# Performance work log

Hardware: AMD Instinct MI355X
Metric: run time of the kernel (lower is better)

## Reference

```python
import jax, jax.numpy as jnp
import numpy as np

EMBED_DIM = 384
N_DOCS = 262144
BATCH = 64
TOP_K = 8
EPS = 1e-8


def setup_inputs() -> dict:
    key = jax.random.key(0)
    kq, kd = jax.random.split(key)
    query = jax.random.normal(kq, (BATCH, EMBED_DIM), dtype=jnp.float32)
    doc_embeddings = jax.random.normal(kd, (N_DOCS, EMBED_DIM), dtype=jnp.float32)
    return {"query": query, "doc_embeddings": doc_embeddings, "top_k": TOP_K}


def reference(query, doc_embeddings, top_k):
    # Cosine similarity: L2-normalize both sides.
    qn = query / (jnp.linalg.norm(query, axis=-1, keepdims=True) + EPS)          # [B, d]
    dn = doc_embeddings / (jnp.linalg.norm(doc_embeddings, axis=-1, keepdims=True) + EPS)  # [N, d]
    # Similarity scores between every query and every document.
    scores = jnp.einsum('bd,nd->bn', qn, dn)                                      # [B, N]
    # Top-k retrieval.
    topk_scores, topk_idx = jax.lax.top_k(scores, top_k)                          # [B, k]
    # Gather retrieved document embeddings.
    retrieved = dn[topk_idx]                                                      # [B, k, d]
    # Context fusion: softmax-weighted sum of retrieved docs.
    weights = jax.nn.softmax(topk_scores, axis=-1)                                # [B, k]
    fused = jnp.einsum('bk,bkd->bd', weights, retrieved)                          # [B, d]
    return fused, topk_scores, topk_idx
```

## Files before the change

kernel.cpp:

```cpp
#include <hip/hip_runtime.h>
#include <math.h>


#define EMBED 384
#define NDOCS 262144
#define BATCH 64
#define TOPK 8
#define DBLK 128
#define NBLK (NDOCS / DBLK)
#define EPSN 1e-8f
#define SC_STRIDE 132

typedef __attribute__((ext_vector_type(8))) short bf16x8;
typedef __attribute__((ext_vector_type(4))) float f32x4;

#define INS8(s_, i_) do {                                                     \
    if ((s_) > ts[7] || ((s_) == ts[7] && (i_) < ti[7])) {                    \
        ts[7] = (s_); ti[7] = (i_);                                           \
        _Pragma("unroll")                                                     \
        for (int r_ = 7; r_ > 0; --r_) {                                      \
            bool sw_ = (ts[r_] > ts[r_-1]) ||                                 \
                       (ts[r_] == ts[r_-1] && ti[r_] < ti[r_-1]);             \
            float a_ = ts[r_-1]; int b_ = ti[r_-1];                           \
            ts[r_-1] = sw_ ? ts[r_] : a_;  ti[r_-1] = sw_ ? ti[r_] : b_;      \
            ts[r_]   = sw_ ? a_ : ts[r_];  ti[r_]   = sw_ ? b_ : ti[r_];      \
        }                                                                     \
    }                                                                         \
} while (0)

__device__ __forceinline__ void split8(float4 f0, float4 f1, bf16x8& bh, bf16x8& bl) {
    float f[8] = {f0.x, f0.y, f0.z, f0.w, f1.x, f1.y, f1.z, f1.w};
#pragma unroll
    for (int i = 0; i < 8; ++i) {
        unsigned u = __float_as_uint(f[i]);
        unsigned h = (u + 0x7fffu + ((u >> 16) & 1u)) >> 16;
        float fh = __uint_as_float(h << 16);
        float r = f[i] - fh;
        unsigned v = __float_as_uint(r);
        unsigned lo = (v + 0x7fffu + ((v >> 16) & 1u)) >> 16;
        bh[i] = (short)h;
        bl[i] = (short)lo;
    }
}

__device__ __forceinline__ float dot8(float4 f0, float4 f1, float s) {
    s = fmaf(f0.x, f0.x, s); s = fmaf(f0.y, f0.y, s);
    s = fmaf(f0.z, f0.z, s); s = fmaf(f0.w, f0.w, s);
    s = fmaf(f1.x, f1.x, s); s = fmaf(f1.y, f1.y, s);
    s = fmaf(f1.z, f1.z, s); s = fmaf(f1.w, f1.w, s);
    return s;
}

__global__ void qprep_kernel(const float* __restrict__ q,
                             unsigned short* __restrict__ qh,
                             unsigned short* __restrict__ ql) {
    const int row = blockIdx.x;
    const int lane = threadIdx.x;
    float v[6];
    float s = 0.f;
#pragma unroll
    for (int i = 0; i < 6; ++i) {
        v[i] = q[row * EMBED + lane + 64 * i];
        s = fmaf(v[i], v[i], s);
    }
#pragma unroll
    for (int off = 32; off > 0; off >>= 1) s += __shfl_xor(s, off);
    float rinv = 1.0f / (sqrtf(s) + EPSN);
#pragma unroll
    for (int i = 0; i < 6; ++i) {
        float f = v[i] * rinv;
        unsigned u = __float_as_uint(f);
        unsigned h = (u + 0x7fffu + ((u >> 16) & 1u)) >> 16;
        float fh = __uint_as_float(h << 16);
        float r = f - fh;
        unsigned vv = __float_as_uint(r);
        unsigned lo = (vv + 0x7fffu + ((vv >> 16) & 1u)) >> 16;
        qh[row * EMBED + lane + 64 * i] = (unsigned short)h;
        ql[row * EMBED + lane + 64 * i] = (unsigned short)lo;
    }
}

__global__ __launch_bounds__(256, 4) void score_topk_kernel(
        const float* __restrict__ docs,
        const unsigned short* __restrict__ qh,
        const unsigned short* __restrict__ ql,
        float* __restrict__ pscore, int* __restrict__ pidx) {
    __shared__ float S[BATCH * SC_STRIDE];

    const int tid = threadIdx.x;
    const int l = tid & 63;
    const int w = tid >> 6;
    const int rowl = l & 15;
    const int koff = (l >> 4) * 8;
    const int d0 = blockIdx.x * DBLK;

    f32x4 acc[2][4];
#pragma unroll
    for (int s = 0; s < 2; ++s)
#pragma unroll
        for (int m = 0; m < 4; ++m) acc[s][m] = (f32x4){0.f, 0.f, 0.f, 0.f};
    float sq0 = 0.f, sq1 = 0.f;

    const float* dp0 = docs + (size_t)(d0 + w * 32 + rowl) * EMBED + koff;
    const float* dp1 = dp0 + 16 * EMBED;
    const unsigned short* qhb = qh + rowl * EMBED + koff;
    const unsigned short* qlb = ql + rowl * EMBED + koff;

    float4 c00 = *(const float4*)dp0, c01 = *(const float4*)(dp0 + 4);
    float4 c10 = *(const float4*)dp1, c11 = *(const float4*)(dp1 + 4);

#define KBODY(kk, PREFETCH)                                                   \
    do {                                                                      \
        bf16x8 ah[4], al[4];                                                  \
        _Pragma("unroll")                                                     \
        for (int m = 0; m < 4; ++m) {                                         \
            ah[m] = *(const bf16x8*)(qhb + m * (16 * EMBED) + (kk));          \
            al[m] = *(const bf16x8*)(qlb + m * (16 * EMBED) + (kk));          \
        }                                                                     \
        float4 n00, n01, n10, n11;                                            \
        if (PREFETCH) {                                                       \
            n00 = *(const float4*)(dp0 + (kk) + 32);                          \
            n01 = *(const float4*)(dp0 + (kk) + 36);                          \
            n10 = *(const float4*)(dp1 + (kk) + 32);                          \
            n11 = *(const float4*)(dp1 + (kk) + 36);                          \
        }                                                                     \
        sq0 = dot8(c00, c01, sq0);                                            \
        sq1 = dot8(c10, c11, sq1);                                            \
        bf16x8 bh0, bl0, bh1, bl1;                                            \
        split8(c00, c01, bh0, bl0);                                           \
        split8(c10, c11, bh1, bl1);                                           \
        _Pragma("unroll")                                                     \
        for (int m = 0; m < 4; ++m)                                           \
            acc[0][m] = __builtin_amdgcn_mfma_f32_16x16x32_bf16(ah[m], bh0, acc[0][m], 0, 0, 0); \
        _Pragma("unroll")                                                     \
        for (int m = 0; m < 4; ++m)                                           \
            acc[1][m] = __builtin_amdgcn_mfma_f32_16x16x32_bf16(ah[m], bh1, acc[1][m], 0, 0, 0); \
        _Pragma("unroll")                                                     \
        for (int m = 0; m < 4; ++m)                                           \
            acc[0][m] = __builtin_amdgcn_mfma_f32_16x16x32_bf16(al[m], bh0, acc[0][m], 0, 0, 0); \
        _Pragma("unroll")                                                     \
        for (int m = 0; m < 4; ++m)                                           \
            acc[1][m] = __builtin_amdgcn_mfma_f32_16x16x32_bf16(al[m], bh1, acc[1][m], 0, 0, 0); \
        _Pragma("unroll")                                                     \
        for (int m = 0; m < 4; ++m)                                           \
            acc[0][m] = __builtin_amdgcn_mfma_f32_16x16x32_bf16(ah[m], bl0, acc[0][m], 0, 0, 0); \
        _Pragma("unroll")                                                     \
        for (int m = 0; m < 4; ++m)                                           \
            acc[1][m] = __builtin_amdgcn_mfma_f32_16x16x32_bf16(ah[m], bl1, acc[1][m], 0, 0, 0); \
        if (PREFETCH) { c00 = n00; c01 = n01; c10 = n10; c11 = n11; }         \
    } while (0)

#pragma unroll 1
    for (int kb = 0; kb < 11; ++kb) {
        KBODY(kb * 32, 1);
    }
    KBODY(352, 0);
#undef KBODY

    {
        float t0 = sq0;
        t0 += __shfl_xor(t0, 16);
        t0 += __shfl_xor(t0, 32);
        float rn0 = 1.0f / (sqrtf(t0) + EPSN);
        float t1 = sq1;
        t1 += __shfl_xor(t1, 16);
        t1 += __shfl_xor(t1, 32);
        float rn1 = 1.0f / (sqrtf(t1) + EPSN);
        const int q0 = (l >> 4) * 4;
#pragma unroll
        for (int m = 0; m < 4; ++m) {
            f32x4 a = acc[0][m];
            const int col0 = w * 32 + rowl;
            S[(m * 16 + q0 + 0) * SC_STRIDE + col0] = a[0] * rn0;
            S[(m * 16 + q0 + 1) * SC_STRIDE + col0] = a[1] * rn0;
            S[(m * 16 + q0 + 2) * SC_STRIDE + col0] = a[2] * rn0;
            S[(m * 16 + q0 + 3) * SC_STRIDE + col0] = a[3] * rn0;
            f32x4 b = acc[1][m];
            const int col1 = w * 32 + 16 + rowl;
            S[(m * 16 + q0 + 0) * SC_STRIDE + col1] = b[0] * rn1;
            S[(m * 16 + q0 + 1) * SC_STRIDE + col1] = b[1] * rn1;
            S[(m * 16 + q0 + 2) * SC_STRIDE + col1] = b[2] * rn1;
            S[(m * 16 + q0 + 3) * SC_STRIDE + col1] = b[3] * rn1;
        }
    }
    __syncthreads();

    float ts[8]; int ti[8];
#pragma unroll
    for (int r = 0; r < 8; ++r) { ts[r] = -3.402823466e38f; ti[r] = 0x7fffffff; }
    const int sq_ = tid & 63, half = tid >> 6;
    if (tid < 128) {
        for (int ii = 0; ii < 64; ++ii) {
            int d = half * 64 + ((ii + sq_) & 63);
            float sc = S[sq_ * SC_STRIDE + d];
            INS8(sc, d0 + d);
        }
    }
    __syncthreads();
    if (half == 1 && tid < 128) {
#pragma unroll
        for (int r = 0; r < 8; ++r) {
            S[sq_ * 8 + r] = ts[r];
            S[512 + sq_ * 8 + r] = __int_as_float(ti[r]);
        }
    }
    __syncthreads();
    if (tid < 64) {
#pragma unroll
        for (int r = 0; r < 8; ++r) {
            float s2 = S[sq_ * 8 + r];
            int i2 = __float_as_int(S[512 + sq_ * 8 + r]);
            INS8(s2, i2);
        }
        size_t o = ((size_t)sq_ * NBLK + blockIdx.x) * TOPK;
        *(float4*)&pscore[o]     = make_float4(ts[0], ts[1], ts[2], ts[3]);
        *(float4*)&pscore[o + 4] = make_float4(ts[4], ts[5], ts[6], ts[7]);
        *(int4*)&pidx[o]     = make_int4(ti[0], ti[1], ti[2], ti[3]);
        *(int4*)&pidx[o + 4] = make_int4(ti[4], ti[5], ti[6], ti[7]);
    }
}

__global__ __launch_bounds__(256) void merge_fuse_kernel(
        const float* __restrict__ docs, const float* __restrict__ pscore,
        const int* __restrict__ pidx, float* __restrict__ out) {
    const int q = blockIdx.x;
    const int tid = threadIdx.x;
    __shared__ float ls[2048];
    __shared__ int   li[2048];
    __shared__ float ls2[512];
    __shared__ int   li2[512];
    __shared__ float ls3[64];
    __shared__ int   li3[64];
    __shared__ int   fi[TOPK];
    __shared__ float wr[TOPK];

    const float* sp = pscore + (size_t)q * (NBLK * TOPK);
    const int*   ip = pidx   + (size_t)q * (NBLK * TOPK);

    float ts[8]; int ti[8];
#pragma unroll
    for (int r = 0; r < 8; ++r) { ts[r] = -3.402823466e38f; ti[r] = 0x7fffffff; }

    for (int i = 0; i < 16; ++i) {
        int c4 = tid + (i << 8);
        float4 s = ((const float4*)sp)[c4];
        if (s.x >= ts[7] || s.y >= ts[7] || s.z >= ts[7] || s.w >= ts[7]) {
            int4 iv = ((const int4*)ip)[c4];
            INS8(s.x, iv.x); INS8(s.y, iv.y); INS8(s.z, iv.z); INS8(s.w, iv.w);
        }
    }
#pragma unroll
    for (int r = 0; r < 8; ++r) { ls[tid * 8 + r] = ts[r]; li[tid * 8 + r] = ti[r]; }
    __syncthreads();

    if (tid < 64) {
#pragma unroll
        for (int r = 0; r < 8; ++r) { ts[r] = -3.402823466e38f; ti[r] = 0x7fffffff; }
        for (int c = 0; c < 32; ++c) {
            int e = tid + c * 64;
            float s = ls[e]; int gi = li[e];
            INS8(s, gi);
        }
#pragma unroll
        for (int r = 0; r < 8; ++r) { ls2[tid * 8 + r] = ts[r]; li2[tid * 8 + r] = ti[r]; }
    }
    __syncthreads();

    if (tid < 8) {
#pragma unroll
        for (int r = 0; r < 8; ++r) { ts[r] = -3.402823466e38f; ti[r] = 0x7fffffff; }
        for (int c = 0; c < 64; ++c) {
            int e = tid + c * 8;
            float s = ls2[e]; int gi = li2[e];
            INS8(s, gi);
        }
#pragma unroll
        for (int r = 0; r < 8; ++r) { ls3[tid * 8 + r] = ts[r]; li3[tid * 8 + r] = ti[r]; }
    }
    __syncthreads();

    if (tid == 0) {
#pragma unroll
        for (int r = 0; r < 8; ++r) { ts[r] = -3.402823466e38f; ti[r] = 0x7fffffff; }
        for (int e = 0; e < 64; ++e) {
            float s = ls3[e]; int gi = li3[e];
            INS8(s, gi);
        }
        float m = ts[0];
        float w[8]; float sum = 0.f;
#pragma unroll
        for (int r = 0; r < 8; ++r) { w[r] = expf(ts[r] - m); sum += w[r]; }
        float rs = 1.0f / sum;
#pragma unroll
        for (int r = 0; r < 8; ++r) {
            fi[r] = ti[r];
            wr[r] = w[r] * rs;
            out[BATCH * EMBED + q * TOPK + r] = ts[r];
            out[BATCH * EMBED + BATCH * TOPK + q * TOPK + r] = (float)ti[r];
        }
    }
    __syncthreads();

    int lane = tid & 63, wave = tid >> 6;
    for (int r = wave; r < TOPK; r += 4) {
        const float* dp = docs + (size_t)fi[r] * EMBED;
        float s = 0.f;
#pragma unroll
        for (int i = 0; i < 6; ++i) { float v = dp[lane + 64 * i]; s = fmaf(v, v, s); }
#pragma unroll
        for (int off = 32; off > 0; off >>= 1) s += __shfl_xor(s, off);
        if (lane == 0) wr[r] = wr[r] / (sqrtf(s) + EPSN);
    }
    __syncthreads();

    for (int dim = tid; dim < EMBED; dim += 256) {
        float a = 0.f;
#pragma unroll
        for (int r = 0; r < 8; ++r)
            a += wr[r] * docs[(size_t)fi[r] * EMBED + dim];
        out[q * EMBED + dim] = a;
    }
}

extern "C" void kernel_launch(void* const* d_in, const int* in_sizes, int n_in,
                              void* d_out, int out_size, void* d_ws, size_t ws_size,
                              hipStream_t stream) {
    const float* query = (const float*)d_in[0];
    const float* docs  = (const float*)d_in[1];
    float* out = (float*)d_out;

    char* ws = (char*)d_ws;
    unsigned short* qh = (unsigned short*)ws;
    unsigned short* ql = (unsigned short*)(ws + 49152);
    float* pscore = (float*)(ws + 98304);
    int*   pidx   = (int*)(ws + 98304 + (size_t)NBLK * BATCH * TOPK * 4);

    qprep_kernel<<<64, 64, 0, stream>>>(query, qh, ql);
    score_topk_kernel<<<NBLK, 256, 0, stream>>>(docs, qh, ql, pscore, pidx);
    merge_fuse_kernel<<<BATCH, 256, 0, stream>>>(docs, pscore, pidx, out);
}
```

Before: 288.1 us.

## Stage doc tiles via async global-to-LDS loads and split top-k merge

The score kernel now streams document tiles into a double-buffered, XOR-swizzled LDS region with global_load_lds. Explicit vmcnt waits let the next k-slice load overlap the split and MFMA work on the current one, and query fragments are fetched with inline-asm global loads. The merge is split into two kernels: 512 blocks each reduce a chunk of partial top-k lists, then a small kernel does the final merge and the weighted fusion. This adds parallelism to the merge stage but costs an extra launch. The hand-tuned waitcnt values and the larger LDS footprint may limit occupancy or correctness if the counts are wrong.

New measurement: 277.7 us. 3.6% less time.

```diff
diff --git a/kernel.cpp b/kernel.cpp
--- a/kernel.cpp
+++ b/kernel.cpp
@@ -28,8 +28,8 @@
     }                                                                         \
 } while (0)
 
-__device__ __forceinline__ void split8(float4 f0, float4 f1, bf16x8& bh, bf16x8& bl) {
-    float f[8] = {f0.x, f0.y, f0.z, f0.w, f1.x, f1.y, f1.z, f1.w};
+__device__ __forceinline__ void split8v(f32x4 f0, f32x4 f1, bf16x8& bh, bf16x8& bl) {
+    float f[8] = {f0[0], f0[1], f0[2], f0[3], f1[0], f1[1], f1[2], f1[3]};
 #pragma unroll
     for (int i = 0; i < 8; ++i) {
         unsigned u = __float_as_uint(f[i]);
@@ -43,12 +43,24 @@
     }
 }
 
-__device__ __forceinline__ float dot8(float4 f0, float4 f1, float s) {
-    s = fmaf(f0.x, f0.x, s); s = fmaf(f0.y, f0.y, s);
-    s = fmaf(f0.z, f0.z, s); s = fmaf(f0.w, f0.w, s);
-    s = fmaf(f1.x, f1.x, s); s = fmaf(f1.y, f1.y, s);
-    s = fmaf(f1.z, f1.z, s); s = fmaf(f1.w, f1.w, s);
+__device__ __forceinline__ float dot8v(f32x4 f0, f32x4 f1, float s) {
+#pragma unroll
+    for (int i = 0; i < 4; ++i) s = fmaf(f0[i], f0[i], s);
+#pragma unroll
+    for (int i = 0; i < 4; ++i) s = fmaf(f1[i], f1[i], s);
     return s;
+}
+
+__device__ __forceinline__ int4 gload16(const void* p) {
+    int4 r;
+    asm volatile("global_load_dwordx4 %0, %1, off" : "=v"(r) : "v"(p) : "memory");
+    return r;
+}
+
+__device__ __forceinline__ f32x4 dsread16(unsigned a) {
+    f32x4 r;
+    asm volatile("ds_read_b128 %0, %1" : "=v"(r) : "v"(a) : "memory");
+    return r;
 }
 
 __global__ void qprep_kernel(const float* __restrict__ q,
@@ -85,13 +97,13 @@
         const unsigned short* __restrict__ qh,
         const unsigned short* __restrict__ ql,
         float* __restrict__ pscore, int* __restrict__ pidx) {
-    __shared__ float S[BATCH * SC_STRIDE];
+    __shared__ __align__(16) char smem[34816];
 
     const int tid = threadIdx.x;
     const int l = tid & 63;
-    const int w = tid >> 6;
+    const int wv = tid >> 6;
     const int rowl = l & 15;
-    const int koff = (l >> 4) * 8;
+    const int ksub = l >> 4;
     const int d0 = blockIdx.x * DBLK;
 
     f32x4 acc[2][4];
@@ -101,62 +113,75 @@
         for (int m = 0; m < 4; ++m) acc[s][m] = (f32x4){0.f, 0.f, 0.f, 0.f};
     float sq0 = 0.f, sq1 = 0.f;
 
-    const float* dp0 = docs + (size_t)(d0 + w * 32 + rowl) * EMBED + koff;
-    const float* dp1 = dp0 + 16 * EMBED;
-    const unsigned short* qhb = qh + rowl * EMBED + koff;
-    const unsigned short* qlb = ql + rowl * EMBED + koff;
-
-    float4 c00 = *(const float4*)dp0, c01 = *(const float4*)(dp0 + 4);
-    float4 c10 = *(const float4*)dp1, c11 = *(const float4*)(dp1 + 4);
-
-#define KBODY(kk, PREFETCH)                                                   \
-    do {                                                                      \
-        bf16x8 ah[4], al[4];                                                  \
-        _Pragma("unroll")                                                     \
-        for (int m = 0; m < 4; ++m) {                                         \
-            ah[m] = *(const bf16x8*)(qhb + m * (16 * EMBED) + (kk));          \
-            al[m] = *(const bf16x8*)(qlb + m * (16 * EMBED) + (kk));          \
-        }                                                                     \
-        float4 n00, n01, n10, n11;                                            \
-        if (PREFETCH) {                                                       \
-            n00 = *(const float4*)(dp0 + (kk) + 32);                          \
-            n01 = *(const float4*)(dp0 + (kk) + 36);                          \
-            n10 = *(const float4*)(dp1 + (kk) + 32);                          \
-            n11 = *(const float4*)(dp1 + (kk) + 36);                          \
-        }                                                                     \
-        sq0 = dot8(c00, c01, sq0);                                            \
-        sq1 = dot8(c10, c11, sq1);                                            \
-        bf16x8 bh0, bl0, bh1, bl1;                                            \
-        split8(c00, c01, bh0, bl0);                                           \
-        split8(c10, c11, bh1, bl1);                                           \
-        _Pragma("unroll")                                                     \
-        for (int m = 0; m < 4; ++m)                                           \
-            acc[0][m] = __builtin_amdgcn_mfma_f32_16x16x32_bf16(ah[m], bh0, acc[0][m], 0, 0, 0); \
-        _Pragma("unroll")                                                     \
-        for (int m = 0; m < 4; ++m)                                           \
-            acc[1][m] = __builtin_amdgcn_mfma_f32_16x16x32_bf16(ah[m], bh1, acc[1][m], 0, 0, 0); \
-        _Pragma("unroll")                                                     \
-        for (int m = 0; m < 4; ++m)                                           \
-            acc[0][m] = __builtin_amdgcn_mfma_f32_16x16x32_bf16(al[m], bh0, acc[0][m], 0, 0, 0); \
-        _Pragma("unroll")                                                     \
-        for (int m = 0; m < 4; ++m)                                           \
-            acc[1][m] = __builtin_amdgcn_mfma_f32_16x16x32_bf16(al[m], bh1, acc[1][m], 0, 0, 0); \
-        _Pragma("unroll")                                                     \
-        for (int m = 0; m < 4; ++m)                                           \
-            acc[0][m] = __builtin_amdgcn_mfma_f32_16x16x32_bf16(ah[m], bl0, acc[0][m], 0, 0, 0); \
-        _Pragma("unroll")                                                     \
-        for (int m = 0; m < 4; ++m)                                           \
-            acc[1][m] = __builtin_amdgcn_mfma_f32_16x16x32_bf16(ah[m], bl1, acc[1][m], 0, 0, 0); \
-        if (PREFETCH) { c00 = n00; c01 = n01; c10 = n10; c11 = n11; }         \
-    } while (0)
+    const float* sgsrc = docs + (size_t)(d0 + wv * 32 + (l >> 3)) * EMBED
+                              + (((l & 7) ^ (l >> 3)) << 2);
+    const unsigned short* qhb = qh + rowl * EMBED + ksub * 8;
+    const unsigned short* qlb = ql + rowl * EMBED + ksub * 8;
+
+    const unsigned bufb = (unsigned)(uintptr_t)smem;
+    const unsigned off00 = wv * 4096 + rowl * 128 + ((ksub * 32 +  0) ^ ((rowl & 7) << 4));
+    const unsigned off01 = wv * 4096 + rowl * 128 + ((ksub * 32 + 16) ^ ((rowl & 7) << 4));
+    const unsigned off10 = off00 + 2048;
+    const unsigned off11 = off01 + 2048;
+
+    {
+        float* db = (float*)smem + wv * 1024;
+#pragma unroll
+        for (int j = 0; j < 4; ++j)
+            __builtin_amdgcn_global_load_lds(sgsrc + j * 3072, db + j * 256, 16, 0, 0);
+    }
+
+#define SCORE_ITER(KB, DO_STAGE, VM1, VM2)                                     \
+    {                                                                          \
+        int4 qr[8];                                                            \
+        _Pragma("unroll")                                                      \
+        for (int m = 0; m < 4; ++m) {                                          \
+            qr[m]     = gload16(qhb + m * (16 * EMBED) + (KB) * 32);           \
+            qr[4 + m] = gload16(qlb + m * (16 * EMBED) + (KB) * 32);           \
+        }                                                                      \
+        if (DO_STAGE) {                                                        \
+            float* db = (float*)(smem + (((KB) + 1) & 1) * 16384) + wv * 1024; \
+            _Pragma("unroll")                                                  \
+            for (int j = 0; j < 4; ++j)                                        \
+                __builtin_amdgcn_global_load_lds(                              \
+                    sgsrc + j * 3072 + ((KB) + 1) * 32, db + j * 256, 16, 0, 0);\
+        }                                                                      \
+        asm volatile("s_waitcnt " VM1 ::: "memory");                           \
+        unsigned pb = bufb + ((KB) & 1) * 16384;                               \
+        f32x4 d00 = dsread16(pb + off00);                                      \
+        f32x4 d01 = dsread16(pb + off01);                                      \
+        f32x4 d10 = dsread16(pb + off10);                                      \
+        f32x4 d11 = dsread16(pb + off11);                                      \
+        asm volatile("s_waitcnt " VM2 " lgkmcnt(0)" ::: "memory");             \
+        __builtin_amdgcn_sched_barrier(0);                                     \
+        sq0 = dot8v(d00, d01, sq0);                                            \
+        sq1 = dot8v(d10, d11, sq1);                                            \
+        bf16x8 bh0, bl0, bh1, bl1;                                             \
+        split8v(d00, d01, bh0, bl0);                                           \
+        split8v(d10, d11, bh1, bl1);                                           \
+        _Pragma("unroll")                                                      \
+        for (int m = 0; m < 4; ++m) {                                          \
+            bf16x8 ah = *(bf16x8*)&qr[m];                                      \
+            bf16x8 al = *(bf16x8*)&qr[4 + m];                                  \
+            acc[0][m] = __builtin_amdgcn_mfma_f32_16x16x32_bf16(ah, bh0, acc[0][m], 0, 0, 0); \
+            acc[1][m] = __builtin_amdgcn_mfma_f32_16x16x32_bf16(ah, bh1, acc[1][m], 0, 0, 0); \
+            acc[0][m] = __builtin_amdgcn_mfma_f32_16x16x32_bf16(al, bh0, acc[0][m], 0, 0, 0); \
+            acc[1][m] = __builtin_amdgcn_mfma_f32_16x16x32_bf16(al, bh1, acc[1][m], 0, 0, 0); \
+            acc[0][m] = __builtin_amdgcn_mfma_f32_16x16x32_bf16(ah, bl0, acc[0][m], 0, 0, 0); \
+            acc[1][m] = __builtin_amdgcn_mfma_f32_16x16x32_bf16(ah, bl1, acc[1][m], 0, 0, 0); \
+        }                                                                      \
+    }
 
 #pragma unroll 1
     for (int kb = 0; kb < 11; ++kb) {
-        KBODY(kb * 32, 1);
-    }
-    KBODY(352, 0);
-#undef KBODY
-
+        SCORE_ITER(kb, 1, "vmcnt(12)", "vmcnt(4)")
+    }
+    SCORE_ITER(11, 0, "vmcnt(8)", "vmcnt(0)")
+#undef SCORE_ITER
+
+    __syncthreads();
+
+    float* S = (float*)smem;
     {
         float t0 = sq0;
         t0 += __shfl_xor(t0, 16);
@@ -166,17 +191,17 @@
         t1 += __shfl_xor(t1, 16);
         t1 += __shfl_xor(t1, 32);
         float rn1 = 1.0f / (sqrtf(t1) + EPSN);
-        const int q0 = (l >> 4) * 4;
+        const int q0 = ksub * 4;
+        const int col0 = wv * 32 + rowl;
+        const int col1 = col0 + 16;
 #pragma unroll
         for (int m = 0; m < 4; ++m) {
             f32x4 a = acc[0][m];
-            const int col0 = w * 32 + rowl;
             S[(m * 16 + q0 + 0) * SC_STRIDE + col0] = a[0] * rn0;
             S[(m * 16 + q0 + 1) * SC_STRIDE + col0] = a[1] * rn0;
             S[(m * 16 + q0 + 2) * SC_STRIDE + col0] = a[2] * rn0;
             S[(m * 16 + q0 + 3) * SC_STRIDE + col0] = a[3] * rn0;
             f32x4 b = acc[1][m];
-            const int col1 = w * 32 + 16 + rowl;
             S[(m * 16 + q0 + 0) * SC_STRIDE + col1] = b[0] * rn1;
             S[(m * 16 + q0 + 1) * SC_STRIDE + col1] = b[1] * rn1;
             S[(m * 16 + q0 + 2) * SC_STRIDE + col1] = b[2] * rn1;
@@ -220,10 +245,11 @@
     }
 }
 
-__global__ __launch_bounds__(256) void merge_fuse_kernel(
-        const float* __restrict__ docs, const float* __restrict__ pscore,
-        const int* __restrict__ pidx, float* __restrict__ out) {
-    const int q = blockIdx.x;
+__global__ __launch_bounds__(256) void merge_a_kernel(
+        const float* __restrict__ pscore, const int* __restrict__ pidx,
+        float* __restrict__ cs, int* __restrict__ ci) {
+    const int q = blockIdx.x >> 3;
+    const int c = blockIdx.x & 7;
     const int tid = threadIdx.x;
     __shared__ float ls[2048];
     __shared__ int   li[2048];
@@ -231,59 +257,76 @@
     __shared__ int   li2[512];
     __shared__ float ls3[64];
     __shared__ int   li3[64];
-    __shared__ int   fi[TOPK];
-    __shared__ float wr[TOPK];
-
-    const float* sp = pscore + (size_t)q * (NBLK * TOPK);
-    const int*   ip = pidx   + (size_t)q * (NBLK * TOPK);
+
+    {
+        size_t o = ((size_t)q * NBLK + c * 256 + tid) * TOPK;
+        float4 s0 = *(const float4*)&pscore[o];
+        float4 s1 = *(const float4*)&pscore[o + 4];
+        int4 i0 = *(const int4*)&pidx[o];
+        int4 i1 = *(const int4*)&pidx[o + 4];
+        ls[tid * 8 + 0] = s0.x; ls[tid * 8 + 1] = s0.y;
+        ls[tid * 8 + 2] = s0.z; ls[tid * 8 + 3] = s0.w;
+        ls[tid * 8 + 4] = s1.x; ls[tid * 8 + 5] = s1.y;
+        ls[tid * 8 + 6] = s1.z; ls[tid * 8 + 7] = s1.w;
+        li[tid * 8 + 0] = i0.x; li[tid * 8 + 1] = i0.y;
+        li[tid * 8 + 2] = i0.z; li[tid * 8 + 3] = i0.w;
+        li[tid * 8 + 4] = i1.x; li[tid * 8 + 5] = i1.y;
+        li[tid * 8 + 6] = i1.z; li[tid * 8 + 7] = i1.w;
+    }
+    __syncthreads();
 
     float ts[8]; int ti[8];
-#pragma unroll
-    for (int r = 0; r < 8; ++r) { ts[r] = -3.402823466e38f; ti[r] = 0x7fffffff; }
-
-    for (int i = 0; i < 16; ++i) {
-        int c4 = tid + (i << 8);
-        float4 s = ((const float4*)sp)[c4];
-        if (s.x >= ts[7] || s.y >= ts[7] || s.z >= ts[7] || s.w >= ts[7]) {
-            int4 iv = ((const int4*)ip)[c4];
-            INS8(s.x, iv.x); INS8(s.y, iv.y); INS8(s.z, iv.z); INS8(s.w, iv.w);
-        }
-    }
-#pragma unroll
-    for (int r = 0; r < 8; ++r) { ls[tid * 8 + r] = ts[r]; li[tid * 8 + r] = ti[r]; }
-    __syncthreads();
-
     if (tid < 64) {
 #pragma unroll
         for (int r = 0; r < 8; ++r) { ts[r] = -3.402823466e38f; ti[r] = 0x7fffffff; }
-        for (int c = 0; c < 32; ++c) {
-            int e = tid + c * 64;
-            float s = ls[e]; int gi = li[e];
+        for (int e = 0; e < 32; ++e) {
+            int k = tid + e * 64;
+            float s = ls[k]; int gi = li[k];
             INS8(s, gi);
         }
 #pragma unroll
         for (int r = 0; r < 8; ++r) { ls2[tid * 8 + r] = ts[r]; li2[tid * 8 + r] = ti[r]; }
     }
     __syncthreads();
-
     if (tid < 8) {
 #pragma unroll
         for (int r = 0; r < 8; ++r) { ts[r] = -3.402823466e38f; ti[r] = 0x7fffffff; }
-        for (int c = 0; c < 64; ++c) {
-            int e = tid + c * 8;
-            float s = ls2[e]; int gi = li2[e];
+        for (int e = 0; e < 64; ++e) {
+            int k = tid + e * 8;
+            float s = ls2[k]; int gi = li2[k];
             INS8(s, gi);
         }
 #pragma unroll
         for (int r = 0; r < 8; ++r) { ls3[tid * 8 + r] = ts[r]; li3[tid * 8 + r] = ti[r]; }
     }
     __syncthreads();
-
     if (tid == 0) {
 #pragma unroll
         for (int r = 0; r < 8; ++r) { ts[r] = -3.402823466e38f; ti[r] = 0x7fffffff; }
         for (int e = 0; e < 64; ++e) {
             float s = ls3[e]; int gi = li3[e];
+            INS8(s, gi);
+        }
+        size_t o = (size_t)(q * 8 + c) * TOPK;
+#pragma unroll
+        for (int r = 0; r < 8; ++r) { cs[o + r] = ts[r]; ci[o + r] = ti[r]; }
+    }
+}
+
+__global__ __launch_bounds__(256) void merge_b_kernel(
+        const float* __restrict__ docs, const float* __restrict__ cs,
+        const int* __restrict__ ci, float* __restrict__ out) {
+    const int q = blockIdx.x;
+    const int tid = threadIdx.x;
+    __shared__ int   fi[TOPK];
+    __shared__ float wr[TOPK];
+
+    if (tid == 0) {
+        float ts[8]; int ti[8];
+#pragma unroll
+        for (int r = 0; r < 8; ++r) { ts[r] = -3.402823466e38f; ti[r] = 0x7fffffff; }
+        for (int e = 0; e < 64; ++e) {
+            float s = cs[q * 64 + e]; int gi = ci[q * 64 + e];
             INS8(s, gi);
         }
         float m = ts[0];
@@ -334,8 +377,12 @@
     unsigned short* ql = (unsigned short*)(ws + 49152);
     float* pscore = (float*)(ws + 98304);
     int*   pidx   = (int*)(ws + 98304 + (size_t)NBLK * BATCH * TOPK * 4);
+    char*  ws3    = ws + 98304 + 2 * (size_t)NBLK * BATCH * TOPK * 4;
+    float* cs     = (float*)ws3;
+    int*   ci     = (int*)(ws3 + BATCH * 8 * TOPK * 4);
 
     qprep_kernel<<<64, 64, 0, stream>>>(query, qh, ql);
     score_topk_kernel<<<NBLK, 256, 0, stream>>>(docs, qh, ql, pscore, pidx);
-    merge_fuse_kernel<<<BATCH, 256, 0, stream>>>(docs, pscore, pidx, out);
-}
+    merge_a_kernel<<<BATCH * 8, 256, 0, stream>>>(pscore, pidx, cs, ci);
+    merge_b_kernel<<<BATCH, 256, 0, stream>>>(docs, cs, ci, out);
+}
```

## Score in single bf16 from pre-swizzled doc copy, rescore top candidates in fp32

Applied to the files above, without the earlier changes.

Replaces the three-term split-bf16 MFMA scoring with a single bf16×bf16 pass. A new conversion kernel first writes docs as a bf16 copy in an MFMA-friendly tiled layout, and the score kernel reads that copy. The merge kernel now keeps 256 candidates per query (top 16 from each of 16 chunks), recomputes their exact fp32 cosine scores from the original docs, and selects the final top-8 from those. This cuts MFMA and conversion work in the hot scoring loop, but adds a full read of the fp32 docs plus a write of a 200MB bf16 copy on every call. It also risks missing true top-k documents if bf16 error pushes them out of the 16-per-block candidate set.

Result: slower. 425.8 us (+47.8%).

```diff
diff --git a/kernel.cpp b/kernel.cpp
--- a/kernel.cpp
+++ b/kernel.cpp
@@ -6,10 +6,9 @@
 #define NDOCS 262144
 #define BATCH 64
 #define TOPK 8
-#define DBLK 128
-#define NBLK (NDOCS / DBLK)
+#define NBLK 2048
 #define EPSN 1e-8f
-#define SC_STRIDE 132
+#define SCW 132
 
 typedef __attribute__((ext_vector_type(8))) short bf16x8;
 typedef __attribute__((ext_vector_type(4))) float f32x4;
@@ -28,32 +27,28 @@
     }                                                                         \
 } while (0)
 
-__device__ __forceinline__ void split8(float4 f0, float4 f1, bf16x8& bh, bf16x8& bl) {
-    float f[8] = {f0.x, f0.y, f0.z, f0.w, f1.x, f1.y, f1.z, f1.w};
-#pragma unroll
-    for (int i = 0; i < 8; ++i) {
-        unsigned u = __float_as_uint(f[i]);
-        unsigned h = (u + 0x7fffu + ((u >> 16) & 1u)) >> 16;
-        float fh = __uint_as_float(h << 16);
-        float r = f[i] - fh;
-        unsigned v = __float_as_uint(r);
-        unsigned lo = (v + 0x7fffu + ((v >> 16) & 1u)) >> 16;
-        bh[i] = (short)h;
-        bl[i] = (short)lo;
-    }
-}
-
-__device__ __forceinline__ float dot8(float4 f0, float4 f1, float s) {
-    s = fmaf(f0.x, f0.x, s); s = fmaf(f0.y, f0.y, s);
-    s = fmaf(f0.z, f0.z, s); s = fmaf(f0.w, f0.w, s);
-    s = fmaf(f1.x, f1.x, s); s = fmaf(f1.y, f1.y, s);
-    s = fmaf(f1.z, f1.z, s); s = fmaf(f1.w, f1.w, s);
-    return s;
+#define INS16(s_, i_) do {                                                    \
+    if ((s_) > ts[15] || ((s_) == ts[15] && (i_) < ti[15])) {                 \
+        ts[15] = (s_); ti[15] = (i_);                                         \
+        _Pragma("unroll")                                                     \
+        for (int r_ = 15; r_ > 0; --r_) {                                     \
+            bool sw_ = (ts[r_] > ts[r_-1]) ||                                 \
+                       (ts[r_] == ts[r_-1] && ti[r_] < ti[r_-1]);             \
+            float a_ = ts[r_-1]; int b_ = ti[r_-1];                           \
+            ts[r_-1] = sw_ ? ts[r_] : a_;  ti[r_-1] = sw_ ? ti[r_] : b_;      \
+            ts[r_]   = sw_ ? a_ : ts[r_];  ti[r_]   = sw_ ? b_ : ti[r_];      \
+        }                                                                     \
+    }                                                                         \
+} while (0)
+
+__device__ __forceinline__ unsigned rne1(float f) {
+    unsigned u = __float_as_uint(f);
+    return (u + 0x7fffu + ((u >> 16) & 1u)) >> 16;
 }
 
 __global__ void qprep_kernel(const float* __restrict__ q,
-                             unsigned short* __restrict__ qh,
-                             unsigned short* __restrict__ ql) {
+                             float* __restrict__ qn,
+                             unsigned short* __restrict__ qhf) {
     const int row = blockIdx.x;
     const int lane = threadIdx.x;
     float v[6];
@@ -68,94 +63,85 @@
     float rinv = 1.0f / (sqrtf(s) + EPSN);
 #pragma unroll
     for (int i = 0; i < 6; ++i) {
+        int k = lane + 64 * i;
         float f = v[i] * rinv;
-        unsigned u = __float_as_uint(f);
-        unsigned h = (u + 0x7fffu + ((u >> 16) & 1u)) >> 16;
-        float fh = __uint_as_float(h << 16);
-        float r = f - fh;
-        unsigned vv = __float_as_uint(r);
-        unsigned lo = (vv + 0x7fffu + ((vv >> 16) & 1u)) >> 16;
-        qh[row * EMBED + lane + 64 * i] = (unsigned short)h;
-        ql[row * EMBED + lane + 64 * i] = (unsigned short)lo;
+        qn[row * EMBED + k] = f;
+        qhf[(row >> 4) * 6144 + (k >> 5) * 512 + ((k >> 3) & 3) * 128
+            + (row & 15) * 8 + (k & 7)] = (unsigned short)rne1(f);
+    }
+}
+
+__global__ __launch_bounds__(256) void conv_kernel(
+        const float* __restrict__ docs, unsigned short* __restrict__ T) {
+    __shared__ __align__(16) uint4 L4[1536];
+    uint2* L2p = (uint2*)L4;
+    const int tid = threadIdx.x;
+
+    for (int p4 = 0; p4 < 4; ++p4) {
+        const int panel = blockIdx.x * 4 + p4;
+        const float4* src = (const float4*)docs + (size_t)panel * 3072;
+        if (p4) __syncthreads();
+#pragma unroll
+        for (int i = 0; i < 12; ++i) {
+            int F = i * 256 + tid;
+            float4 v = src[F];
+            int dd = (F * 10923) >> 20;
+            int r4 = F - dd * 96;
+            uint2 hv;
+            hv.x = rne1(v.x) | (rne1(v.y) << 16);
+            hv.y = rne1(v.z) | (rne1(v.w) << 16);
+            unsigned byte_off = (unsigned)((r4 >> 3) * 2048 + (dd >> 4) * 1024
+                              + ((r4 >> 1) & 3) * 256 + (dd & 15) * 16
+                              + (r4 & 1) * 8);
+            L2p[byte_off >> 3] = hv;
+        }
+        __syncthreads();
+        uint4* dst = (uint4*)((char*)T + (size_t)panel * 24576);
+#pragma unroll
+        for (int j = 0; j < 6; ++j)
+            dst[j * 256 + tid] = L4[j * 256 + tid];
     }
 }
 
 __global__ __launch_bounds__(256, 4) void score_topk_kernel(
-        const float* __restrict__ docs,
-        const unsigned short* __restrict__ qh,
-        const unsigned short* __restrict__ ql,
+        const unsigned short* __restrict__ T,
+        const unsigned short* __restrict__ qhf,
         float* __restrict__ pscore, int* __restrict__ pidx) {
-    __shared__ float S[BATCH * SC_STRIDE];
+    __shared__ float S[BATCH * SCW];
 
     const int tid = threadIdx.x;
     const int l = tid & 63;
     const int w = tid >> 6;
-    const int rowl = l & 15;
-    const int koff = (l >> 4) * 8;
-    const int d0 = blockIdx.x * DBLK;
+    const int d0 = blockIdx.x * 128;
+
+    const char* Tb = (const char*)T + (size_t)(blockIdx.x * 4 + w) * 24576 + l * 16;
+    const char* Qb = (const char*)qhf + l * 16;
 
     f32x4 acc[2][4];
 #pragma unroll
-    for (int s = 0; s < 2; ++s)
-#pragma unroll
-        for (int m = 0; m < 4; ++m) acc[s][m] = (f32x4){0.f, 0.f, 0.f, 0.f};
+    for (int dt = 0; dt < 2; ++dt)
+#pragma unroll
+        for (int qt = 0; qt < 4; ++qt) acc[dt][qt] = (f32x4){0.f, 0.f, 0.f, 0.f};
     float sq0 = 0.f, sq1 = 0.f;
 
-    const float* dp0 = docs + (size_t)(d0 + w * 32 + rowl) * EMBED + koff;
-    const float* dp1 = dp0 + 16 * EMBED;
-    const unsigned short* qhb = qh + rowl * EMBED + koff;
-    const unsigned short* qlb = ql + rowl * EMBED + koff;
-
-    float4 c00 = *(const float4*)dp0, c01 = *(const float4*)(dp0 + 4);
-    float4 c10 = *(const float4*)dp1, c11 = *(const float4*)(dp1 + 4);
-
-#define KBODY(kk, PREFETCH)                                                   \
-    do {                                                                      \
-        bf16x8 ah[4], al[4];                                                  \
-        _Pragma("unroll")                                                     \
-        for (int m = 0; m < 4; ++m) {                                         \
-            ah[m] = *(const bf16x8*)(qhb + m * (16 * EMBED) + (kk));          \
-            al[m] = *(const bf16x8*)(qlb + m * (16 * EMBED) + (kk));          \
-        }                                                                     \
-        float4 n00, n01, n10, n11;                                            \
-        if (PREFETCH) {                                                       \
-            n00 = *(const float4*)(dp0 + (kk) + 32);                          \
-            n01 = *(const float4*)(dp0 + (kk) + 36);                          \
-            n10 = *(const float4*)(dp1 + (kk) + 32);                          \
-            n11 = *(const float4*)(dp1 + (kk) + 36);                          \
-        }                                                                     \
-        sq0 = dot8(c00, c01, sq0);                                            \
-        sq1 = dot8(c10, c11, sq1);                                            \
-        bf16x8 bh0, bl0, bh1, bl1;                                            \
-        split8(c00, c01, bh0, bl0);                                           \
-        split8(c10, c11, bh1, bl1);                                           \
-        _Pragma("unroll")                                                     \
-        for (int m = 0; m < 4; ++m)                                           \
-            acc[0][m] = __builtin_amdgcn_mfma_f32_16x16x32_bf16(ah[m], bh0, acc[0][m], 0, 0, 0); \
-        _Pragma("unroll")                                                     \
-        for (int m = 0; m < 4; ++m)                                           \
-            acc[1][m] = __builtin_amdgcn_mfma_f32_16x16x32_bf16(ah[m], bh1, acc[1][m], 0, 0, 0); \
-        _Pragma("unroll")                                                     \
-        for (int m = 0; m < 4; ++m)                                           \
-            acc[0][m] = __builtin_amdgcn_mfma_f32_16x16x32_bf16(al[m], bh0, acc[0][m], 0, 0, 0); \
-        _Pragma("unroll")                                                     \
-        for (int m = 0; m < 4; ++m)                                           \
-            acc[1][m] = __builtin_amdgcn_mfma_f32_16x16x32_bf16(al[m], bh1, acc[1][m], 0, 0, 0); \
-        _Pragma("unroll")                                                     \
-        for (int m = 0; m < 4; ++m)                                           \
-            acc[0][m] = __builtin_amdgcn_mfma_f32_16x16x32_bf16(ah[m], bl0, acc[0][m], 0, 0, 0); \
-        _Pragma("unroll")                                                     \
-        for (int m = 0; m < 4; ++m)                                           \
-            acc[1][m] = __builtin_amdgcn_mfma_f32_16x16x32_bf16(ah[m], bl1, acc[1][m], 0, 0, 0); \
-        if (PREFETCH) { c00 = n00; c01 = n01; c10 = n10; c11 = n11; }         \
-    } while (0)
-
-#pragma unroll 1
-    for (int kb = 0; kb < 11; ++kb) {
-        KBODY(kb * 32, 1);
-    }
-    KBODY(352, 0);
-#undef KBODY
+#pragma unroll
+    for (int kb = 0; kb < 12; ++kb) {
+        bf16x8 b0 = *(const bf16x8*)(Tb + kb * 2048);
+        bf16x8 b1 = *(const bf16x8*)(Tb + kb * 2048 + 1024);
+#pragma unroll
+        for (int e = 0; e < 8; ++e) {
+            float f0 = __uint_as_float(((unsigned)(unsigned short)b0[e]) << 16);
+            float f1 = __uint_as_float(((unsigned)(unsigned short)b1[e]) << 16);
+            sq0 = fmaf(f0, f0, sq0);
+            sq1 = fmaf(f1, f1, sq1);
+        }
+#pragma unroll
+        for (int qt = 0; qt < 4; ++qt) {
+            bf16x8 a = *(const bf16x8*)(Qb + qt * 12288 + kb * 1024);
+            acc[0][qt] = __builtin_amdgcn_mfma_f32_16x16x32_bf16(a, b0, acc[0][qt], 0, 0, 0);
+            acc[1][qt] = __builtin_amdgcn_mfma_f32_16x16x32_bf16(a, b1, acc[1][qt], 0, 0, 0);
+        }
+    }
 
     {
         float t0 = sq0;
@@ -167,20 +153,20 @@
         t1 += __shfl_xor(t1, 32);
         float rn1 = 1.0f / (sqrtf(t1) + EPSN);
         const int q0 = (l >> 4) * 4;
-#pragma unroll
-        for (int m = 0; m < 4; ++m) {
-            f32x4 a = acc[0][m];
-            const int col0 = w * 32 + rowl;
-            S[(m * 16 + q0 + 0) * SC_STRIDE + col0] = a[0] * rn0;
-            S[(m * 16 + q0 + 1) * SC_STRIDE + col0] = a[1] * rn0;
-            S[(m * 16 + q0 + 2) * SC_STRIDE + col0] = a[2] * rn0;
-            S[(m * 16 + q0 + 3) * SC_STRIDE + col0] = a[3] * rn0;
-            f32x4 b = acc[1][m];
-            const int col1 = w * 32 + 16 + rowl;
-            S[(m * 16 + q0 + 0) * SC_STRIDE + col1] = b[0] * rn1;
-            S[(m * 16 + q0 + 1) * SC_STRIDE + col1] = b[1] * rn1;
-            S[(m * 16 + q0 + 2) * SC_STRIDE + col1] = b[2] * rn1;
-            S[(m * 16 + q0 + 3) * SC_STRIDE + col1] = b[3] * rn1;
+        const int col0 = w * 32 + (l & 15);
+        const int col1 = col0 + 16;
+#pragma unroll
+        for (int qt = 0; qt < 4; ++qt) {
+            f32x4 a = acc[0][qt];
+            S[(qt * 16 + q0 + 0) * SCW + col0] = a[0] * rn0;
+            S[(qt * 16 + q0 + 1) * SCW + col0] = a[1] * rn0;
+            S[(qt * 16 + q0 + 2) * SCW + col0] = a[2] * rn0;
+            S[(qt * 16 + q0 + 3) * SCW + col0] = a[3] * rn0;
+            f32x4 b = acc[1][qt];
+            S[(qt * 16 + q0 + 0) * SCW + col1] = b[0] * rn1;
+            S[(qt * 16 + q0 + 1) * SCW + col1] = b[1] * rn1;
+            S[(qt * 16 + q0 + 2) * SCW + col1] = b[2] * rn1;
+            S[(qt * 16 + q0 + 3) * SCW + col1] = b[3] * rn1;
         }
     }
     __syncthreads();
@@ -192,7 +178,7 @@
     if (tid < 128) {
         for (int ii = 0; ii < 64; ++ii) {
             int d = half * 64 + ((ii + sq_) & 63);
-            float sc = S[sq_ * SC_STRIDE + d];
+            float sc = S[sq_ * SCW + d];
             INS8(sc, d0 + d);
         }
     }
@@ -220,96 +206,115 @@
     }
 }
 
-__global__ __launch_bounds__(256) void merge_fuse_kernel(
-        const float* __restrict__ docs, const float* __restrict__ pscore,
-        const int* __restrict__ pidx, float* __restrict__ out) {
+__global__ __launch_bounds__(256) void rescore_kernel(
+        const float* __restrict__ docs, const float* __restrict__ qn,
+        const float* __restrict__ pscore, const int* __restrict__ pidx,
+        float* __restrict__ out) {
     const int q = blockIdx.x;
     const int tid = threadIdx.x;
-    __shared__ float ls[2048];
-    __shared__ int   li[2048];
-    __shared__ float ls2[512];
-    __shared__ int   li2[512];
-    __shared__ float ls3[64];
-    __shared__ int   li3[64];
+    __shared__ float s1[4096];
+    __shared__ int   i1[4096];
+    __shared__ int   cand[256];
+    __shared__ float cs2[256];
+    __shared__ float cn2[256];
     __shared__ int   fi[TOPK];
     __shared__ float wr[TOPK];
 
-    const float* sp = pscore + (size_t)q * (NBLK * TOPK);
-    const int*   ip = pidx   + (size_t)q * (NBLK * TOPK);
-
-    float ts[8]; int ti[8];
-#pragma unroll
-    for (int r = 0; r < 8; ++r) { ts[r] = -3.402823466e38f; ti[r] = 0x7fffffff; }
-
-    for (int i = 0; i < 16; ++i) {
-        int c4 = tid + (i << 8);
-        float4 s = ((const float4*)sp)[c4];
-        if (s.x >= ts[7] || s.y >= ts[7] || s.z >= ts[7] || s.w >= ts[7]) {
-            int4 iv = ((const int4*)ip)[c4];
-            INS8(s.x, iv.x); INS8(s.y, iv.y); INS8(s.z, iv.z); INS8(s.w, iv.w);
-        }
-    }
-#pragma unroll
-    for (int r = 0; r < 8; ++r) { ls[tid * 8 + r] = ts[r]; li[tid * 8 + r] = ti[r]; }
-    __syncthreads();
-
-    if (tid < 64) {
-#pragma unroll
-        for (int r = 0; r < 8; ++r) { ts[r] = -3.402823466e38f; ti[r] = 0x7fffffff; }
-        for (int c = 0; c < 32; ++c) {
-            int e = tid + c * 64;
-            float s = ls[e]; int gi = li[e];
-            INS8(s, gi);
-        }
-#pragma unroll
-        for (int r = 0; r < 8; ++r) { ls2[tid * 8 + r] = ts[r]; li2[tid * 8 + r] = ti[r]; }
-    }
-    __syncthreads();
-
-    if (tid < 8) {
-#pragma unroll
-        for (int r = 0; r < 8; ++r) { ts[r] = -3.402823466e38f; ti[r] = 0x7fffffff; }
-        for (int c = 0; c < 64; ++c) {
-            int e = tid + c * 8;
-            float s = ls2[e]; int gi = li2[e];
-            INS8(s, gi);
-        }
-#pragma unroll
-        for (int r = 0; r < 8; ++r) { ls3[tid * 8 + r] = ts[r]; li3[tid * 8 + r] = ti[r]; }
+    {
+        float ts[16]; int ti[16];
+#pragma unroll
+        for (int r = 0; r < 16; ++r) { ts[r] = -3.402823466e38f; ti[r] = 0x7fffffff; }
+        const int c = tid >> 4, j = tid & 15;
+        const float* sp = pscore + (size_t)q * 16384 + c * 1024 + j;
+        const int*   ip = pidx   + (size_t)q * 16384 + c * 1024 + j;
+        for (int ii = 0; ii < 64; ++ii) {
+            float s = sp[ii * 16];
+            if (s > ts[15] || (s == ts[15])) {
+                int gi = ip[ii * 16];
+                INS16(s, gi);
+            }
+        }
+#pragma unroll
+        for (int r = 0; r < 16; ++r) { s1[tid * 16 + r] = ts[r]; i1[tid * 16 + r] = ti[r]; }
+    }
+    __syncthreads();
+
+    if (tid < 16) {
+        float ts[16]; int ti[16];
+#pragma unroll
+        for (int r = 0; r < 16; ++r) { ts[r] = -3.402823466e38f; ti[r] = 0x7fffffff; }
+        for (int t16 = 0; t16 < 16; ++t16) {
+            int base = (tid * 16 + t16) * 16;
+            if (s1[base] < ts[15]) continue;
+            for (int r2 = 0; r2 < 16; ++r2) {
+                float s = s1[base + r2]; int gi = i1[base + r2];
+                INS16(s, gi);
+            }
+        }
+#pragma unroll
+        for (int r = 0; r < 16; ++r) cand[tid * 16 + r] = ti[r];
+    }
+    __syncthreads();
+
+    {
+        const int l = tid & 63, w = tid >> 6;
+        float qr[6];
+#pragma unroll
+        for (int i = 0; i < 6; ++i) qr[i] = qn[q * EMBED + l + 64 * i];
+        for (int cc = 0; cc < 64; ++cc) {
+            int cd = w * 64 + cc;
+            int id = cand[cd];
+            const float* dp = docs + (size_t)id * EMBED;
+            float dot = 0.f, ss = 0.f;
+#pragma unroll
+            for (int i = 0; i < 6; ++i) {
+                float v = dp[l + 64 * i];
+                dot = fmaf(v, qr[i], dot);
+                ss = fmaf(v, v, ss);
+            }
+#pragma unroll
+            for (int off = 32; off > 0; off >>= 1) {
+                dot += __shfl_xor(dot, off);
+                ss  += __shfl_xor(ss, off);
+            }
+            if (l == 0) {
+                float rn = 1.0f / (sqrtf(ss) + EPSN);
+                cs2[cd] = dot * rn;
+                cn2[cd] = rn;
+            }
+        }
     }
     __syncthreads();
 
     if (tid == 0) {
-#pragma unroll
-        for (int r = 0; r < 8; ++r) { ts[r] = -3.402823466e38f; ti[r] = 0x7fffffff; }
-        for (int e = 0; e < 64; ++e) {
-            float s = ls3[e]; int gi = li3[e];
-            INS8(s, gi);
+        float ts[8]; int ti[8]; int tp[8];
+#pragma unroll
+        for (int r = 0; r < 8; ++r) { ts[r] = -3.402823466e38f; ti[r] = 0x7fffffff; tp[r] = 0; }
+        for (int e = 0; e < 256; ++e) {
+            float s = cs2[e]; int id = cand[e];
+            if (s > ts[7] || (s == ts[7] && id < ti[7])) {
+                ts[7] = s; ti[7] = id; tp[7] = e;
+#pragma unroll
+                for (int r = 7; r > 0; --r) {
+                    bool sw = (ts[r] > ts[r-1]) || (ts[r] == ts[r-1] && ti[r] < ti[r-1]);
+                    float a = ts[r-1]; int b = ti[r-1]; int p = tp[r-1];
+                    ts[r-1] = sw ? ts[r] : a;  ti[r-1] = sw ? ti[r] : b;  tp[r-1] = sw ? tp[r] : p;
+                    ts[r]   = sw ? a : ts[r];  ti[r]   = sw ? b : ti[r];  tp[r]   = sw ? p : tp[r];
+                }
+            }
         }
         float m = ts[0];
-        float w[8]; float sum = 0.f;
-#pragma unroll
-        for (int r = 0; r < 8; ++r) { w[r] = expf(ts[r] - m); sum += w[r]; }
+        float wv[8]; float sum = 0.f;
+#pragma unroll
+        for (int r = 0; r < 8; ++r) { wv[r] = expf(ts[r] - m); sum += wv[r]; }
         float rs = 1.0f / sum;
 #pragma unroll
         for (int r = 0; r < 8; ++r) {
             fi[r] = ti[r];
-            wr[r] = w[r] * rs;
+            wr[r] = wv[r] * rs * cn2[tp[r]];
             out[BATCH * EMBED + q * TOPK + r] = ts[r];
             out[BATCH * EMBED + BATCH * TOPK + q * TOPK + r] = (float)ti[r];
         }
-    }
-    __syncthreads();
-
-    int lane = tid & 63, wave = tid >> 6;
-    for (int r = wave; r < TOPK; r += 4) {
-        const float* dp = docs + (size_t)fi[r] * EMBED;
-        float s = 0.f;
-#pragma unroll
-        for (int i = 0; i < 6; ++i) { float v = dp[lane + 64 * i]; s = fmaf(v, v, s); }
-#pragma unroll
-        for (int off = 32; off > 0; off >>= 1) s += __shfl_xor(s, off);
-        if (lane == 0) wr[r] = wr[r] / (sqrtf(s) + EPSN);
     }
     __syncthreads();
 
@@ -330,12 +335,14 @@
     float* out = (float*)d_out;
 
     char* ws = (char*)d_ws;
-    unsigned short* qh = (unsigned short*)ws;
-    unsigned short* ql = (unsigned short*)(ws + 49152);
-    float* pscore = (float*)(ws + 98304);
-    int*   pidx   = (int*)(ws + 98304 + (size_t)NBLK * BATCH * TOPK * 4);
-
-    qprep_kernel<<<64, 64, 0, stream>>>(query, qh, ql);
-    score_topk_kernel<<<NBLK, 256, 0, stream>>>(docs, qh, ql, pscore, pidx);
-    merge_fuse_kernel<<<BATCH, 256, 0, stream>>>(docs, pscore, pidx, out);
-}
+    unsigned short* qhf = (unsigned short*)ws;
+    float* qn  = (float*)(ws + 49152);
+    unsigned short* T = (unsigned short*)(ws + 147456);
+    float* pscore = (float*)(ws + 147456 + 201326592ull);
+    int*   pidx   = (int*)(ws + 147456 + 201326592ull + 4194304ull);
+
+    qprep_kernel<<<64, 64, 0, stream>>>(query, qn, qhf);
+    conv_kernel<<<2048, 256, 0, stream>>>(docs, T);
+    score_topk_kernel<<<NBLK, 256, 0, stream>>>(T, qhf, pscore, pidx);
+    rescore_kernel<<<BATCH, 256, 0, stream>>>(docs, qn, pscore, pidx, out);
+}
```
